# Kernel tuning notes

Hardware: AMD Instinct MI355X
Metric: run time of the kernel (lower is better)

Reference implementation:

```python
import jax, jax.numpy as jnp
import numpy as np

EMB, HID, GNN_LAYERS, N_CLASS = 1024, 300, 4, 7
B, N = 64, 64
NEG = 1e30  # mask_logic constant from the original repo


def _gru_cell(x, h, wih, whh, bih, bhh):
    # PyTorch nn.GRUCell math
    gi = x @ wih.T + bih
    gh = h @ whh.T + bhh
    i_r, i_z, i_n = jnp.split(gi, 3, axis=-1)
    h_r, h_z, h_n = jnp.split(gh, 3, axis=-1)
    r = jax.nn.sigmoid(i_r + h_r)
    z = jax.nn.sigmoid(i_z + h_z)
    n = jnp.tanh(i_n + r * h_n)
    return (1.0 - z) * n + z * h


def _build_adj_smask(speakers):
    # Vectorized get_adj_mask: utterance i attends to k in [last_same_speaker(i), i-1]
    Bz, Nu = speakers.shape
    idx = jnp.arange(Nu)
    lower = idx[None, :] < idx[:, None]                              # (N,N): k < i
    same = speakers[:, :, None] == speakers[:, None, :]              # (B,N,N)
    prev_same = same & lower[None]
    last = jnp.max(jnp.where(prev_same, idx[None, None, :], -1), axis=-1)  # (B,N)
    start = jnp.maximum(last, 0)                                     # no prior same speaker -> from 0
    valid = speakers >= 0
    adj = lower[None] & (idx[None, None, :] >= start[:, :, None]) & valid[:, :, None]
    s_mask = same & valid[:, :, None] & valid[:, None, :]
    return adj.astype(jnp.float32), s_mask.astype(jnp.float32)


def _run_layer(Hin, adj, s_mask, wq, wk, b, wr0, wr1,
               wih_c, whh_c, bih_c, bhh_c, wih_p, whh_p, bih_p, bhh_p):
    # Sequential DAG update: H1[i] = GRUc(Hin[i], M) + GRUp(M, Hin[i]),
    # M = GAT attention of Hin[i] over already-computed H1[:i].
    Bz, Nu, D = Hin.shape
    x0 = Hin[:, 0]
    z = jnp.zeros_like(x0)
    C0 = _gru_cell(x0, z, wih_c, whh_c, bih_c, bhh_c)
    P0 = _gru_cell(z, x0, wih_p, whh_p, bih_p, bhh_p)
    H1 = jnp.zeros_like(Hin).at[:, 0].set(C0 + P0)

    @jax.checkpoint
    def step(H1, inp):
        Q, a, sm, i = inp                           # Q:(B,D)  a,sm:(B,N)
        # GAT score: Linear(cat(Q,K)) split into query/key parts
        alpha = (Q @ wq)[:, None] + H1 @ wk + b      # (B,N)
        alpha = alpha - (1.0 - a) * NEG              # mask_logic (positions >= i have a=0)
        w = jax.nn.softmax(alpha, axis=-1)           # (B,N)
        V = (H1 @ wr0.T) * sm[..., None] + (H1 @ wr1.T) * (1.0 - sm[..., None])
        M = jnp.einsum('bn,bnd->bd', w, V)           # (B,D)
        C = _gru_cell(Q, M, wih_c, whh_c, bih_c, bhh_c)
        P = _gru_cell(M, Q, wih_p, whh_p, bih_p, bhh_p)
        return H1.at[:, i].set(C + P), None

    xs = (jnp.moveaxis(Hin, 1, 0)[1:], jnp.moveaxis(adj, 1, 0)[1:],
          jnp.moveaxis(s_mask, 1, 0)[1:], jnp.arange(1, Nu))
    H1, _ = jax.lax.scan(step, H1, xs)
    return H1


def setup_inputs() -> dict:
    key = jax.random.key(0)
    ks = iter(jax.random.split(key, 40))
    def rn(shape, s=0.02):
        return jax.random.normal(next(ks), shape, jnp.float32) * s
    L = GNN_LAYERS
    in_dim = HID * (L + 1) + EMB
    return dict(
        features=jax.random.normal(next(ks), (B, N, EMB), jnp.float32),
        speakers=jax.random.randint(next(ks), (B, N), 0, 2, jnp.int32),
        w_in=rn((HID, EMB)), b_in=jnp.zeros((HID,), jnp.float32),
        gat_wq=rn((L, HID)), gat_wk=rn((L, HID)), gat_b=jnp.zeros((L,), jnp.float32),
        wr0=rn((L, HID, HID)), wr1=rn((L, HID, HID)),
        wih_c=rn((L, 3 * HID, HID)), whh_c=rn((L, 3 * HID, HID)),
        bih_c=jnp.zeros((L, 3 * HID), jnp.float32), bhh_c=jnp.zeros((L, 3 * HID), jnp.float32),
        wih_p=rn((L, 3 * HID, HID)), whh_p=rn((L, 3 * HID, HID)),
        bih_p=jnp.zeros((L, 3 * HID), jnp.float32), bhh_p=jnp.zeros((L, 3 * HID), jnp.float32),
        w1=rn((HID, in_dim)), b1=jnp.zeros((HID,), jnp.float32),
        w2=rn((HID, HID)), b2=jnp.zeros((HID,), jnp.float32),
        w3=rn((N_CLASS, HID)), b3=jnp.zeros((N_CLASS,), jnp.float32),
    )


def reference(features, speakers, w_in, b_in, gat_wq, gat_wk, gat_b, wr0, wr1,
              wih_c, whh_c, bih_c, bhh_c, wih_p, whh_p, bih_p, bhh_p,
              w1, b1, w2, b2, w3, b3):
    adj, s_mask = _build_adj_smask(speakers)
    H0 = jax.nn.relu(features @ w_in.T + b_in)          # (B,N,HID)
    Hs = [H0]
    Hin = H0
    for l in range(GNN_LAYERS):
        Hin = _run_layer(Hin, adj, s_mask, gat_wq[l], gat_wk[l], gat_b[l],
                         wr0[l], wr1[l], wih_c[l], whh_c[l], bih_c[l], bhh_c[l],
                         wih_p[l], whh_p[l], bih_p[l], bhh_p[l])
        Hs.append(Hin)
    Hs.append(features)
    Hcat = jnp.concatenate(Hs, axis=2)                  # (B,N,HID*(L+1)+EMB)
    h = jax.nn.relu(Hcat @ w1.T + b1)
    h = jax.nn.relu(h @ w2.T + b2)                      # dropout is identity in eval
    logits = h @ w3.T + b3                              # (B,N,N_CLASS)
    return logits
```

## Files before the change

kernel.cpp:

```cpp
#include <hip/hip_runtime.h>
#include <hip/hip_bf16.h>

typedef _Float16 f16x2 __attribute__((ext_vector_type(2)));

#define HID 300
#define NSEQ 64
#define NROWS 4096

union U { uint4 u; f16x2 h[4]; };

__device__ __forceinline__ float sigm(float x){ return 1.f/(1.f+__expf(-x)); }

__device__ __forceinline__ float fdot2a(f16x2 a, f16x2 b, float c){
#if __has_builtin(__builtin_amdgcn_fdot2)
  return __builtin_amdgcn_fdot2(a, b, c, false);
#else
  return c + (float)a.x*(float)b.x + (float)a.y*(float)b.y;
#endif
}

__device__ __forceinline__ void xstore(float* p, float v){
  __hip_atomic_store(p, v, __ATOMIC_RELAXED, __HIP_MEMORY_SCOPE_AGENT);
}
__device__ __forceinline__ float xload(const float* p){
  return __hip_atomic_load(p, __ATOMIC_RELAXED, __HIP_MEMORY_SCOPE_AGENT);
}
__device__ __forceinline__ int xloadi(const int* p){
  return __hip_atomic_load(p, __ATOMIC_RELAXED, __HIP_MEMORY_SCOPE_AGENT);
}

#define NSYNC (3*32*16 + 3*128*2*16 + 64)

__global__ void convert_all_kernel(
    const float* __restrict__ whh_c, const float* __restrict__ wih_p,
    const float* __restrict__ wih_c, const float* __restrict__ whh_p,
    const float* __restrict__ wr0,   const float* __restrict__ wr1,
    const float* __restrict__ w_in,  const float* __restrict__ w1,
    const float* __restrict__ w2,
    f16x2* __restrict__ W_M4, f16x2* __restrict__ WrT4, f16x2* __restrict__ W_P4,
    f16x2* __restrict__ W_H4, f16x2* __restrict__ W_14, f16x2* __restrict__ W_24,
    int* __restrict__ syncc)
{
  const int NA = 4*38*1800*4;
  const int NB = 4*38*600*4;
  const int NP = 4*38*1800*4;
  const int NH = 128*300*4;
  const int N1 = 318*304*4;
  const int N2 = 38*304*4;
  const int NS = NSYNC;
  const int TOT = NA+NB+NP+NH+N1+N2+NS;
  for (int idx0 = blockIdx.x*blockDim.x + threadIdx.x; idx0 < TOT; idx0 += gridDim.x*blockDim.x){
    int idx = idx0;
    if (idx < NA){
      int l    = idx/(38*1800*4);
      int rem  = idx - l*(38*1800*4);
      int kg   = rem/(1800*4);
      int rem2 = rem - kg*(1800*4);
      int o = rem2>>2, s = rem2&3;
      int c = (kg*4+s)*2;
      float v0=0.f, v1=0.f;
      if (c < 300){
        const float* src = (o<900) ? (whh_c + ((size_t)l*900+o)*300)
                                   : (wih_p + ((size_t)l*900+(o-900))*300);
        v0 = src[c]; v1 = src[c+1];
      }
      f16x2 t; t.x=(_Float16)v0; t.y=(_Float16)v1;
      W_M4[idx] = t; continue;
    }
    idx -= NA;
    if (idx < NB){
      int l    = idx/(38*600*4);
      int rem  = idx - l*(38*600*4);
      int kg   = rem/(600*4);
      int rem2 = rem - kg*(600*4);
      int t6 = rem2>>2, s = rem2&3;
      int d = t6>>1, hh = t6&1;
      int c = (kg*4+s)*2;
      float v0=0.f, v1=0.f;
      if (c < 300){
        const float* src = hh ? (wr1 + ((size_t)l*300+d)*300)
                              : (wr0 + ((size_t)l*300+d)*300);
        v0 = src[c]; v1 = src[c+1];
      }
      f16x2 t; t.x=(_Float16)v0; t.y=(_Float16)v1;
      WrT4[idx] = t; continue;
    }
    idx -= NB;
    if (idx < NP){
      int l    = idx/(38*1800*4);
      int rem  = idx - l*(38*1800*4);
      int kg   = rem/(1800*4);
      int rem2 = rem - kg*(1800*4);
      int o = rem2>>2, s = rem2&3;
      int c = (kg*4+s)*2;
      float v0=0.f, v1=0.f;
      if (c < 300){
        const float* src = (o<900) ? (wih_c + ((size_t)l*900+o)*300)
                                   : (whh_p + ((size_t)l*900+(o-900))*300);
        v0 = src[c]; v1 = src[c+1];
      }
      f16x2 t; t.x=(_Float16)v0; t.y=(_Float16)v1;
      W_P4[idx] = t; continue;
    }
    idx -= NP;
    if (idx < NH){
      int kg  = idx/(300*4);
      int rem = idx - kg*(300*4);
      int o = rem>>2, s = rem&3;
      int c = (kg*4+s)*2;
      f16x2 t; t.x=(_Float16)w_in[(size_t)o*1024+c]; t.y=(_Float16)w_in[(size_t)o*1024+c+1];
      W_H4[idx] = t; continue;
    }
    idx -= NH;
    if (idx < N1){
      int kgg = idx/(304*4);
      int rem = idx - kgg*(304*4);
      int o = rem>>2, s = rem&3;
      int segbase, seglen, kgl;
      if (kgg < 190){ int seg = kgg/38; kgl = kgg - seg*38; segbase = seg*300; seglen = 300; }
      else { int kk = kgg-190; int sf = kk>>6; kgl = kk&63; segbase = 1500 + sf*512; seglen = 512; }
      int c = (kgl*4+s)*2;
      float v0=0.f, v1=0.f;
      if (o < 300 && c < seglen){
        v0 = w1[(size_t)o*2524 + segbase + c];
        if (c+1 < seglen) v1 = w1[(size_t)o*2524 + segbase + c + 1];
      }
      f16x2 t; t.x=(_Float16)v0; t.y=(_Float16)v1;
      W_14[idx] = t; continue;
    }
    idx -= N1;
    if (idx < N2){
      int kg = idx/(304*4);
      int rem = idx - kg*(304*4);
      int o = rem>>2, s = rem&3;
      int c = (kg*4+s)*2;
      float v0=0.f, v1=0.f;
      if (o < 300 && c < 300){ v0 = w2[(size_t)o*300+c]; v1 = w2[(size_t)o*300+c+1]; }
      f16x2 t; t.x=(_Float16)v0; t.y=(_Float16)v1;
      W_24[idx] = t; continue;
    }
    idx -= N2;
    syncc[idx] = 0;
  }
}

__global__ __launch_bounds__(256) void h0_kernel(const float* __restrict__ feat,
    const f16x2* __restrict__ WH, const float* __restrict__ b_in, float* __restrict__ H0)
{
  const int tid = threadIdx.x;
  const int r0  = blockIdx.x*8;
  __shared__ f16x2 X[8][512];
  for (int t=tid; t<8*512; t+=256){
    int r=t>>9, p=t&511, c=2*p;
    f16x2 h; h.x=(_Float16)feat[(size_t)(r0+r)*1024+c];
    h.y=(_Float16)feat[(size_t)(r0+r)*1024+c+1];
    X[r][p]=h;
  }
  __syncthreads();
  const uint4* WHu = (const uint4*)WH;
  const int o0 = tid, o1 = tid+256;
  const bool h1v = (o1 < 300);
  float acc[2][8];
  #pragma unroll
  for (int j=0;j<2;j++)
    #pragma unroll
    for (int r=0;r<8;r++) acc[j][r]=0.f;
  for (int kg=0; kg<128; kg++){
    U w0, w1;
    w0.u = WHu[(size_t)kg*300 + o0];
    if (h1v) w1.u = WHu[(size_t)kg*300 + o1];
    #pragma unroll
    for (int r=0;r<8;r++){
      const f16x2* xp = &X[r][kg*4];
      f16x2 x0=xp[0],x1=xp[1],x2=xp[2],x3=xp[3];
      acc[0][r] = fdot2a(w0.h[3],x3, fdot2a(w0.h[2],x2, fdot2a(w0.h[1],x1, fdot2a(w0.h[0],x0, acc[0][r]))));
      if (h1v)
        acc[1][r] = fdot2a(w1.h[3],x3, fdot2a(w1.h[2],x2, fdot2a(w1.h[1],x1, fdot2a(w1.h[0],x0, acc[1][r]))));
    }
  }
  {
    float bb = b_in[o0];
    #pragma unroll
    for (int r=0;r<8;r++) H0[(size_t)(r0+r)*HID + o0] = fmaxf(acc[0][r]+bb, 0.f);
  }
  if (h1v){
    float bb = b_in[o1];
    #pragma unroll
    for (int r=0;r<8;r++) H0[(size_t)(r0+r)*HID + o1] = fmaxf(acc[1][r]+bb, 0.f);
  }
}

__global__ __launch_bounds__(1024) void scan_pipe_kernel(
  float* __restrict__ Hball,
  const f16x2* __restrict__ W_M4, const f16x2* __restrict__ WrT4, const f16x2* __restrict__ W_P4,
  const float* __restrict__ bih_c, const float* __restrict__ bhh_c,
  const float* __restrict__ bih_p, const float* __restrict__ bhh_p,
  const float* __restrict__ gwq, const float* __restrict__ gwk, const float* __restrict__ gbv,
  const int* __restrict__ speakers, float* __restrict__ xrow, int* __restrict__ syncc,
  float* __restrict__ xhEx)
{
  (void)gwq; (void)gbv;
  __shared__ _Float16 Hh[2][NSEQ][304];
  __shared__ float pre_s[2][1800];
  __shared__ float gates[2][1800];
  __shared__ float Mf[2][304];
  __shared__ f16x2 Mh[2][152];
  __shared__ f16x2 u01h[2][304];
  __shared__ float wgt[2][NSEQ];
  __shared__ float kd[2][NSEQ];
  __shared__ float red[2][320];
  __shared__ float xf[2][304];
  __shared__ f16x2 xh[2][152];
  __shared__ int   spk[2][NSEQ];
  __shared__ int   startA[2][NSEQ];
  __shared__ int   sLayer, sPair, sHalf;

  const int tid = threadIdx.x;

  if (tid == 0){
    int xcc = 0;
    asm volatile("s_getreg_b32 %0, hwreg(HW_REG_XCC_ID)" : "=s"(xcc));
    int pref = (xcc >> 1) & 3;
    int* claimc = syncc + 3*32*16 + 3*128*2*16;
    int l = 0, p = 0, hf = 0;
    #pragma unroll 1
    for (int t=0; t<4; ++t){
      int cand = (pref + t) & 3;
      int idx = __hip_atomic_fetch_add(&claimc[cand*16], 1, __ATOMIC_RELAXED, __HIP_MEMORY_SCOPE_AGENT);
      if (idx < 64){ l = cand; p = idx>>1; hf = idx&1; break; }
    }
    sLayer = l; sPair = p; sHalf = hf;
  }
  __syncthreads();
  const int layer = sLayer;
  const int pair  = sPair;
  const int hf    = sHalf;
  const int base0 = (2*pair)*NSEQ;
  const int base1 = (2*pair+1)*NSEQ;

  const uint4* Wm4 = (const uint4*)(W_M4 + (size_t)layer*38*1800*4);
  const uint4* Wr4 = (const uint4*)(WrT4 + (size_t)layer*38*600*4);
  const uint4* Wp4 = (const uint4*)(W_P4 + (size_t)layer*38*1800*4);
  const float* HinB0 = Hball + (size_t)base0*300;
  const float* HinB1 = Hball + (size_t)base1*300;
  float* HoutB0 = Hball + ((size_t)(layer+1)*NROWS + (size_t)base0)*300;
  float* HoutB1 = Hball + ((size_t)(layer+1)*NROWS + (size_t)base1)*300;
  int* cntP = syncc + (layer*32 + pair)*16;
  int* cntC = (layer>0) ? (syncc + ((layer-1)*32 + pair)*16) : (int*)0;
  const float* xin  = xrow + (size_t)(((layer-1)*32 + pair)*2)*NSEQ*300;
  float*       xout = xrow + (size_t)((layer*32 + pair)*2)*NSEQ*300;

  const int lp = layer*32 + pair;
  float* xhMy = xhEx + ((size_t)lp*2 + hf)*600;
  const float* xhPt = xhEx + ((size_t)lp*2 + (1-hf))*600;
  int* fEmy = syncc + 1536 + (lp*2 + hf)*16;
  const int* fEpt = syncc + 1536 + (lp*2 + (1-hf))*16;

  const int w  = tid >> 6;
  const int rc = tid >> 9;
  const int rt = tid & 511;

  float bcr=0,bcz=0,bcn=0,bpr=0,bpz=0,bpn=0,wkv=0;
  if (rt < 150){
    const int de = hf*150 + rt;
    bcr=bhh_c[layer*900+de]; bcz=bhh_c[layer*900+300+de]; bcn=bhh_c[layer*900+600+de];
    bpr=bih_p[layer*900+de]; bpz=bih_p[layer*900+300+de]; bpn=bih_p[layer*900+600+de];
    wkv=gwk[layer*300+de];
  }
  float wkp=0;
  if (tid < 300){
    const int r = (tid<150)? tid : (tid-150);
    wkp = gwk[layer*300 + (1-hf)*150 + r];
  }

  int opm = 0; float ppb = 0.f;
  if (tid < 900){
    const int g = tid/150;
    const int dd = tid - g*150;
    opm = g*300 + hf*150 + dd;
    ppb = (opm<900) ? bih_c[layer*900+opm] : bhh_p[layer*900+(opm-900)];
  }

  if (tid < 64) spk[0][tid] = speakers[base0+tid];
  else if (tid < 128) spk[1][tid-64] = speakers[base1+(tid-64)];
  for (int t=tid; t<2*1800; t+=1024) ((float*)gates)[t]=0.f;
  for (int t=tid; t<2*304; t+=1024) ((float*)Mf)[t]=0.f;
  if (tid >= 128 && tid < 168){ int t=tid-128; red[t/20][300+(t%20)] = 0.f; }
  if (tid >= 168 && tid < 176){ int t=tid-168; xf[t>>2][300+(t&3)] = 0.f; }
  if (tid >= 176 && tid < 180){
    int t=tid-176; f16x2 z; z.x=(_Float16)0.f; z.y=(_Float16)0.f;
    Mh[t>>1][150+(t&1)]=z; xh[t>>1][150+(t&1)]=z;
    u01h[t>>1][150+(t&1)]=z; u01h[t>>1][302+(t&1)]=z;
  }
  __syncthreads();
  if (tid < 64){
    int s=0; for (int j=tid-1;j>=0;--j) if (spk[0][j]==spk[0][tid]){s=j;break;}
    startA[0][tid]=s;
  } else if (tid < 128){
    int t=tid-64;
    int s=0; for (int j=t-1;j>=0;--j) if (spk[1][j]==spk[1][t]){s=j;break;}
    startA[1][t]=s;
  }
  if (layer>0 && tid==0){
    while (xloadi(cntC) < 2) __builtin_amdgcn_s_sleep(8);
  }
  __syncthreads();

  for (int i=0; i<NSEQ; ++i){
    if (rt < 150){
      float x0, x1;
      if (layer==0){
        const float* Hin = rc ? HinB1 : HinB0;
        float2 v = *(const float2*)(Hin + (size_t)i*300 + 2*rt);
        x0=v.x; x1=v.y;
      } else {
        const float* xi = xin + (size_t)rc*NSEQ*300 + (size_t)i*300;
        x0 = xload(xi + 2*rt);
        x1 = xload(xi + 2*rt + 1);
      }
      xf[rc][2*rt]=x0; xf[rc][2*rt+1]=x1;
      f16x2 h; h.x=(_Float16)x0; h.y=(_Float16)x1; xh[rc][rt]=h;
    }
    __syncthreads();
    if (tid < 900){
      float aA0=0,aA1=0,aA2=0,aA3=0, aB0=0,aB1=0,aB2=0,aB3=0;
      for (int kg=0;kg<38;kg++){
        U v; v.u = Wp4[(size_t)kg*1800 + opm];
        f16x2 xA0=xh[0][kg*4+0],xA1=xh[0][kg*4+1],xA2=xh[0][kg*4+2],xA3=xh[0][kg*4+3];
        f16x2 xB0=xh[1][kg*4+0],xB1=xh[1][kg*4+1],xB2=xh[1][kg*4+2],xB3=xh[1][kg*4+3];
        aA0=fdot2a(v.h[0],xA0,aA0); aA1=fdot2a(v.h[1],xA1,aA1);
        aA2=fdot2a(v.h[2],xA2,aA2); aA3=fdot2a(v.h[3],xA3,aA3);
        aB0=fdot2a(v.h[0],xB0,aB0); aB1=fdot2a(v.h[1],xB1,aB1);
        aB2=fdot2a(v.h[2],xB2,aB2); aB3=fdot2a(v.h[3],xB3,aB3);
      }
      pre_s[0][opm] = (aA0+aA1)+(aA2+aA3) + ppb;
      pre_s[1][opm] = (aB0+aB1)+(aB2+aB3) + ppb;
    }
    __syncthreads();
    if (i > 0){
      if (tid==0){
        while (xloadi(fEpt) < i) __builtin_amdgcn_s_sleep(1);
      }
      __syncthreads();
      if (tid < 300){
        const int c = (tid<150)? 0 : 1;
        const int r = tid - c*150;
        const int pd = (1-hf)*150 + r;
        float hv = xload(xhPt + ((i-1)&1)*300 + c*150 + r);
        red[c][pd] = hv * wkp;
        Hh[c][i-1][pd] = (_Float16)hv;
      }
      __syncthreads();
      if (w==0 || w==8){
        const int c = (w==8);
        const int lane = tid & 63;
        float s = red[c][lane]+red[c][lane+64]+red[c][lane+128]+red[c][lane+192]+red[c][lane+256];
        #pragma unroll
        for (int o=32;o>0;o>>=1) s += __shfl_xor(s,o);
        if (lane==0) kd[c][i-1]=s;
        {
          const int st = startA[c][i];
          const bool in = (lane>=st) && (lane<i);
          float kv = (lane==i-1) ? s : kd[c][lane];
          float a = in ? kv : -3.0e38f;
          float m = a;
          #pragma unroll
          for (int o=32;o>0;o>>=1) m = fmaxf(m,__shfl_xor(m,o));
          float e = in ? __expf(a-m) : 0.f;
          float ss = e;
          #pragma unroll
          for (int o=32;o>0;o>>=1) ss += __shfl_xor(ss,o);
          wgt[c][lane] = e/ss;
        }
      }
      __syncthreads();
      #pragma unroll 1
      for (int pass=0; pass<2; ++pass){
        int T = tid + pass*1024;
        if (T < 1200){
          const int c = (T >= 600);
          const int t = T - c*600;
          const int d  = (t<300)? t : (t-300);
          const int wh = (t>=300);
          const int st = startA[c][i]; const int ms = spk[c][i];
          float u=0.f;
          for (int j=st;j<i;++j){
            float sel = ((spk[c][j]==ms) != (wh!=0)) ? 1.f : 0.f;
            u += sel*wgt[c][j]*(float)Hh[c][j][d];
          }
          ((_Float16*)&u01h[c][0])[(wh?304:0) + d] = (_Float16)u;
        }
      }
      __syncthreads();
      if (tid < 600){
        const int hh = tid&1;
        const f16x2* uA = (const f16x2*)&u01h[0][0] + hh*152;
        const f16x2* uB = (const f16x2*)&u01h[1][0] + hh*152;
        float a0=0,a1=0,a2=0,a3=0, b0=0,b1=0,b2=0,b3=0;
        for (int kg=0;kg<38;kg++){
          U v; v.u = Wr4[(size_t)kg*600 + tid];
          a0=fdot2a(v.h[0],uA[kg*4+0],a0); a1=fdot2a(v.h[1],uA[kg*4+1],a1);
          a2=fdot2a(v.h[2],uA[kg*4+2],a2); a3=fdot2a(v.h[3],uA[kg*4+3],a3);
          b0=fdot2a(v.h[0],uB[kg*4+0],b0); b1=fdot2a(v.h[1],uB[kg*4+1],b1);
          b2=fdot2a(v.h[2],uB[kg*4+2],b2); b3=fdot2a(v.h[3],uB[kg*4+3],b3);
        }
        float aA = (a0+a1)+(a2+a3);
        float aB = (b0+b1)+(b2+b3);
        float m2A = aA + __shfl_xor(aA,1);
        float m2B = aB + __shfl_xor(aB,1);
        if ((tid&1)==0){ Mf[0][tid>>1] = m2A; Mf[1][tid>>1] = m2B; }
        float moA = __shfl_xor(m2A,2);
        float moB = __shfl_xor(m2B,2);
        if ((tid&3)==0){
          f16x2 hA; hA.x=(_Float16)m2A; hA.y=(_Float16)moA; Mh[0][tid>>2]=hA;
          f16x2 hB; hB.x=(_Float16)m2B; hB.y=(_Float16)moB; Mh[1][tid>>2]=hB;
        }
      }
      __syncthreads();
      if (tid < 900){
        float aA0=0,aA1=0,aA2=0,aA3=0, aB0=0,aB1=0,aB2=0,aB3=0;
        for (int kg=0;kg<38;kg++){
          U v; v.u = Wm4[(size_t)kg*1800 + opm];
          f16x2 mA0=Mh[0][kg*4+0], mA1=Mh[0][kg*4+1], mA2=Mh[0][kg*4+2], mA3=Mh[0][kg*4+3];
          f16x2 mB0=Mh[1][kg*4+0], mB1=Mh[1][kg*4+1], mB2=Mh[1][kg*4+2], mB3=Mh[1][kg*4+3];
          aA0=fdot2a(v.h[0],mA0,aA0); aA1=fdot2a(v.h[1],mA1,aA1);
          aA2=fdot2a(v.h[2],mA2,aA2); aA3=fdot2a(v.h[3],mA3,aA3);
          aB0=fdot2a(v.h[0],mB0,aB0); aB1=fdot2a(v.h[1],mB1,aB1);
          aB2=fdot2a(v.h[2],mB2,aB2); aB3=fdot2a(v.h[3],mB3,aB3);
        }
        gates[0][opm] = (aA0+aA1)+(aA2+aA3);
        gates[1][opm] = (aB0+aB1)+(aB2+aB3);
      }
      __syncthreads();
    }
    if (rt < 150){
      const int de = hf*150 + rt;
      const float M = Mf[rc][de];
      const float* ps = pre_s[rc];
      const float* gs = gates[rc];
      float r  = sigm(ps[de] + gs[de] + bcr);
      float z  = sigm(ps[300+de] + gs[300+de] + bcz);
      float n  = tanhf(ps[600+de] + r*(gs[600+de]+bcn));
      float C  = (1.f-z)*n + z*M;
      float rp = sigm(gs[900+de]+bpr + ps[900+de]);
      float zp = sigm(gs[1200+de]+bpz + ps[1200+de]);
      float np = tanhf(gs[1500+de]+bpn + rp*ps[1500+de]);
      float qv = xf[rc][de];
      float P  = (1.f-zp)*np + zp*qv;
      float h  = C + P;
      Hh[rc][i][de] = (_Float16)h;
      red[rc][de] = h*wkv;
      float* Ho = rc ? HoutB1 : HoutB0;
      Ho[(size_t)i*300 + de] = h;
      xstore(xhMy + (i&1)*300 + rc*150 + rt, h);
      if (layer<3) xstore(xout + (size_t)rc*NSEQ*300 + (size_t)i*300 + de, h);
    }
    asm volatile("s_waitcnt vmcnt(0)" ::: "memory");
    __syncthreads();
    if (tid==0){
      __hip_atomic_fetch_add(fEmy, 1, __ATOMIC_RELAXED, __HIP_MEMORY_SCOPE_AGENT);
      if (layer<3) __hip_atomic_fetch_add(cntP, 1, __ATOMIC_RELAXED, __HIP_MEMORY_SCOPE_AGENT);
      if (layer>0 && i<63){
        while (xloadi(cntC) < 2*(i+2)) __builtin_amdgcn_s_sleep(8);
      }
    }
    __syncthreads();
  }
}

__global__ __launch_bounds__(256) void head_kernel(
  const float* __restrict__ H0, const float* __restrict__ Hl1,
  const float* __restrict__ Hl2, const float* __restrict__ Hl3,
  const float* __restrict__ Hl4, const float* __restrict__ feat,
  const f16x2* __restrict__ W14, const float* __restrict__ b1,
  const f16x2* __restrict__ W24, const float* __restrict__ b2,
  const float* __restrict__ w3, const float* __restrict__ b3,
  float* __restrict__ out)
{
  const int tid = threadIdx.x;
  const int r0  = blockIdx.x*16;
  __shared__ f16x2 Xh[16*256];
  __shared__ _Float16 h1h[16*304];
  __shared__ float S2[16*304];
  const uint4* W14u = (const uint4*)W14;
  const uint4* W24u = (const uint4*)W24;

  float acc0[16], acc1[16];
  #pragma unroll
  for (int r=0;r<16;r++){ acc0[r]=0.f; acc1[r]=0.f; }
  const int o  = tid;
  const int o2 = tid + 256;
  const bool has2 = (o2 < 300);

  #pragma unroll
  for (int seg=0; seg<7; seg++){
    const float* src = (seg==0)?H0:(seg==1)?Hl1:(seg==2)?Hl2:(seg==3)?Hl3:(seg==4)?Hl4:feat;
    if (seg < 5){
      for (int t=tid; t<16*152; t+=256){
        int r=t/152, p=t-r*152, c=2*p;
        float v0 = (c<300)? src[(size_t)(r0+r)*300 + c] : 0.f;
        float v1 = (c+1<300)? src[(size_t)(r0+r)*300 + c+1] : 0.f;
        f16x2 h; h.x=(_Float16)v0; h.y=(_Float16)v1;
        Xh[r*256+p] = h;
      }
    } else {
      const int cb = (seg-5)*512;
      for (int t=tid; t<16*256; t+=256){
        int r=t>>8, p=t&255;
        float v0 = src[(size_t)(r0+r)*1024 + cb + 2*p];
        float v1 = src[(size_t)(r0+r)*1024 + cb + 2*p+1];
        f16x2 h; h.x=(_Float16)v0; h.y=(_Float16)v1;
        Xh[r*256+p] = h;
      }
    }
    __syncthreads();
    const int kgs = (seg<5)?38:64;
    const int kgo = (seg<5)? seg*38 : 190+(seg-5)*64;
    if (o < 300){
      for (int kg=0; kg<kgs; kg++){
        U a, b;
        a.u = W14u[(size_t)(kgo+kg)*304 + o];
        if (has2) b.u = W14u[(size_t)(kgo+kg)*304 + o2];
        #pragma unroll
        for (int r=0;r<16;r++){
          const f16x2* xp = &Xh[r*256 + kg*4];
          float t0 = fdot2a(a.h[0], xp[0], 0.f);
          t0 = fdot2a(a.h[1], xp[1], t0);
          t0 = fdot2a(a.h[2], xp[2], t0);
          t0 = fdot2a(a.h[3], xp[3], t0);
          acc0[r] += t0;
          if (has2){
            float t1 = fdot2a(b.h[0], xp[0], 0.f);
            t1 = fdot2a(b.h[1], xp[1], t1);
            t1 = fdot2a(b.h[2], xp[2], t1);
            t1 = fdot2a(b.h[3], xp[3], t1);
            acc1[r] += t1;
          }
        }
      }
    }
    __syncthreads();
  }
  if (o < 300){
    float bb = b1[o];
    #pragma unroll
    for (int r=0;r<16;r++) h1h[r*304+o] = (_Float16)fmaxf(acc0[r]+bb, 0.f);
  }
  if (has2){
    float bb = b1[o2];
    #pragma unroll
    for (int r=0;r<16;r++) h1h[r*304+o2] = (_Float16)fmaxf(acc1[r]+bb, 0.f);
  }
  if (tid < 4){
    #pragma unroll
    for (int r=0;r<16;r++) h1h[r*304+300+tid] = (_Float16)0.f;
  }
  __syncthreads();
  #pragma unroll
  for (int r=0;r<16;r++){ acc0[r]=0.f; acc1[r]=0.f; }
  if (o < 300){
    for (int kg=0; kg<38; kg++){
      U a, b;
      a.u = W24u[(size_t)kg*304 + o];
      if (has2) b.u = W24u[(size_t)kg*304 + o2];
      #pragma unroll
      for (int r=0;r<16;r++){
        const f16x2* xp = (const f16x2*)&h1h[r*304] + kg*4;
        float t0 = fdot2a(a.h[0], xp[0], 0.f);
        t0 = fdot2a(a.h[1], xp[1], t0);
        t0 = fdot2a(a.h[2], xp[2], t0);
        t0 = fdot2a(a.h[3], xp[3], t0);
        acc0[r] += t0;
        if (has2){
          float t1 = fdot2a(b.h[0], xp[0], 0.f);
          t1 = fdot2a(b.h[1], xp[1], t1);
          t1 = fdot2a(b.h[2], xp[2], t1);
          t1 = fdot2a(b.h[3], xp[3], t1);
          acc1[r] += t1;
        }
      }
    }
  }
  __syncthreads();
  if (o < 300){
    float bb = b2[o];
    #pragma unroll
    for (int r=0;r<16;r++) S2[r*304+o] = fmaxf(acc0[r]+bb, 0.f);
  }
  if (has2){
    float bb = b2[o2];
    #pragma unroll
    for (int r=0;r<16;r++) S2[r*304+o2] = fmaxf(acc1[r]+bb, 0.f);
  }
  __syncthreads();
  if (tid < 16*7){
    int r = tid/7, c = tid - r*7;
    float s = b3[c];
    const float* wrow = w3 + (size_t)c*HID;
    for (int k=0;k<300;k++) s += wrow[k]*S2[r*304+k];
    out[(size_t)(r0+r)*7 + c] = s;
  }
}

extern "C" void kernel_launch(void* const* d_in, const int* in_sizes, int n_in,
                              void* d_out, int out_size, void* d_ws, size_t ws_size,
                              hipStream_t stream)
{
  (void)in_sizes; (void)n_in; (void)out_size; (void)ws_size;
  const float* feat  = (const float*)d_in[0];
  const int*   spk   = (const int*)d_in[1];
  const float* w_in  = (const float*)d_in[2];
  const float* b_in  = (const float*)d_in[3];
  const float* gwq   = (const float*)d_in[4];
  const float* gwk   = (const float*)d_in[5];
  const float* gb    = (const float*)d_in[6];
  const float* wr0   = (const float*)d_in[7];
  const float* wr1   = (const float*)d_in[8];
  const float* wih_c = (const float*)d_in[9];
  const float* whh_c = (const float*)d_in[10];
  const float* bih_c = (const float*)d_in[11];
  const float* bhh_c = (const float*)d_in[12];
  const float* wih_p = (const float*)d_in[13];
  const float* whh_p = (const float*)d_in[14];
  const float* bih_p = (const float*)d_in[15];
  const float* bhh_p = (const float*)d_in[16];
  const float* w1    = (const float*)d_in[17];
  const float* b1    = (const float*)d_in[18];
  const float* w2    = (const float*)d_in[19];
  const float* b2    = (const float*)d_in[20];
  const float* w3    = (const float*)d_in[21];
  const float* b3    = (const float*)d_in[22];
  float* out = (float*)d_out;

  char* ws = (char*)d_ws;
  size_t off = 0;
  auto alloc = [&](size_t bytes)->void*{
    void* p = ws + off;
    off += (bytes + 255) & ~(size_t)255;
    return p;
  };
  f16x2* W_M4 = (f16x2*)alloc((size_t)4*38*1800*4 * sizeof(f16x2));
  f16x2* WrT4 = (f16x2*)alloc((size_t)4*38*600*4  * sizeof(f16x2));
  f16x2* W_P4 = (f16x2*)alloc((size_t)4*38*1800*4 * sizeof(f16x2));
  f16x2* W_H4 = (f16x2*)alloc((size_t)128*300*4   * sizeof(f16x2));
  f16x2* W_14 = (f16x2*)alloc((size_t)318*304*4   * sizeof(f16x2));
  f16x2* W_24 = (f16x2*)alloc((size_t)38*304*4    * sizeof(f16x2));
  float* Hball = (float*)alloc((size_t)5*NROWS*HID*sizeof(float));
  float* xrow  = (float*)alloc((size_t)3*64*NSEQ*HID*sizeof(float));
  int*   syncc = (int*)alloc((size_t)NSYNC*sizeof(int));
  float* xhEx  = (float*)alloc((size_t)128*2*600*sizeof(float));

  {
    const int tot = 4*38*1800*4 + 4*38*600*4 + 4*38*1800*4 + 128*300*4
                  + 318*304*4 + 38*304*4 + NSYNC;
    convert_all_kernel<<<(tot+255)/256, 256, 0, stream>>>(whh_c, wih_p, wih_c, whh_p,
        wr0, wr1, w_in, w1, w2, W_M4, WrT4, W_P4, W_H4, W_14, W_24, syncc);
  }
  h0_kernel<<<NROWS/8, 256, 0, stream>>>(feat, W_H4, b_in, Hball);

  scan_pipe_kernel<<<256, 1024, 0, stream>>>(Hball, W_M4, WrT4, W_P4,
      bih_c, bhh_c, bih_p, bhh_p, gwq, gwk, gb, spk, xrow, syncc, xhEx);

  head_kernel<<<NROWS/16, 256, 0, stream>>>(
      Hball, Hball + (size_t)NROWS*HID, Hball + (size_t)2*NROWS*HID,
      Hball + (size_t)3*NROWS*HID, Hball + (size_t)4*NROWS*HID,
      feat, W_14, b1, W_24, b2, w3, b3, out);
}
```

Baseline: 1.792 ms.

## Overlap partner handoff and attention softmax with input-projection GEMV via warp specialization

Warps 0 and 8 are dedicated to spinning on the partner-half flag, loading the exchanged hidden values, computing key scores and the masked softmax. The other 14 warps compute the input projection at the same time, and 4 leftover projection outputs are assigned to lanes of warp 0. This removes two block-wide barriers per sequence step and hides the cross-block wait behind the projection GEMV. In exchange, warp 0 now carries extra projection work, which may lengthen the critical path, and the spin-wait is done by whole wavefronts.

```diff
diff --git a/kernel.cpp b/kernel.cpp
--- a/kernel.cpp
+++ b/kernel.cpp
@@ -256,9 +256,10 @@
   int* fEmy = syncc + 1536 + (lp*2 + hf)*16;
   const int* fEpt = syncc + 1536 + (lp*2 + (1-hf))*16;
 
-  const int w  = tid >> 6;
-  const int rc = tid >> 9;
-  const int rt = tid & 511;
+  const int w    = tid >> 6;
+  const int rc   = tid >> 9;
+  const int rt   = tid & 511;
+  const int lane = tid & 63;
 
   float bcr=0,bcz=0,bcn=0,bpr=0,bpz=0,bpn=0,wkv=0;
   if (rt < 150){
@@ -267,18 +268,35 @@
     bpr=bih_p[layer*900+de]; bpz=bih_p[layer*900+300+de]; bpn=bih_p[layer*900+600+de];
     wkv=gwk[layer*300+de];
   }
-  float wkp=0;
-  if (tid < 300){
-    const int r = (tid<150)? tid : (tid-150);
-    wkp = gwk[layer*300 + (1-hf)*150 + r];
-  }
-
-  int opm = 0; float ppb = 0.f;
+  float wkp0=0, wkp1=0, wkp2=0;
+  if (w==0 || w==8){
+    const int pbase = layer*300 + (1-hf)*150;
+    wkp0 = gwk[pbase + lane];
+    wkp1 = gwk[pbase + 64 + lane];
+    if (lane < 22) wkp2 = gwk[pbase + 128 + lane];
+  }
+
+  const bool isP = (w != 0) && (w != 8);
+  int opmP = 0; float ppbP = 0.f;
+  if (isP){
+    const int pidx = (tid < 512) ? (tid - 64) : (tid - 128);
+    const int g = pidx/150;
+    const int dd = pidx - g*150;
+    opmP = g*300 + hf*150 + dd;
+    ppbP = (opmP<900) ? bih_c[layer*900+opmP] : bhh_p[layer*900+(opmP-900)];
+  }
+  int opmX = 0; float ppbX = 0.f;
+  if (w==0 && lane<4){
+    const int rr = 896 + lane;
+    opmX = 1500 + hf*150 + (rr - 750);
+    ppbX = (opmX<900) ? bih_c[layer*900+opmX] : bhh_p[layer*900+(opmX-900)];
+  }
+
+  int opm = 0;
   if (tid < 900){
     const int g = tid/150;
     const int dd = tid - g*150;
     opm = g*300 + hf*150 + dd;
-    ppb = (opm<900) ? bih_c[layer*900+opm] : bhh_p[layer*900+(opm-900)];
   }
 
   if (tid < 64) spk[0][tid] = speakers[base0+tid];
@@ -322,10 +340,11 @@
       f16x2 h; h.x=(_Float16)x0; h.y=(_Float16)x1; xh[rc][rt]=h;
     }
     __syncthreads();
-    if (tid < 900){
+
+    if (isP){
       float aA0=0,aA1=0,aA2=0,aA3=0, aB0=0,aB1=0,aB2=0,aB3=0;
       for (int kg=0;kg<38;kg++){
-        U v; v.u = Wp4[(size_t)kg*1800 + opm];
+        U v; v.u = Wp4[(size_t)kg*1800 + opmP];
         f16x2 xA0=xh[0][kg*4+0],xA1=xh[0][kg*4+1],xA2=xh[0][kg*4+2],xA3=xh[0][kg*4+3];
         f16x2 xB0=xh[1][kg*4+0],xB1=xh[1][kg*4+1],xB2=xh[1][kg*4+2],xB3=xh[1][kg*4+3];
         aA0=fdot2a(v.h[0],xA0,aA0); aA1=fdot2a(v.h[1],xA1,aA1);
@@ -333,47 +352,55 @@
         aB0=fdot2a(v.h[0],xB0,aB0); aB1=fdot2a(v.h[1],xB1,aB1);
         aB2=fdot2a(v.h[2],xB2,aB2); aB3=fdot2a(v.h[3],xB3,aB3);
       }
-      pre_s[0][opm] = (aA0+aA1)+(aA2+aA3) + ppb;
-      pre_s[1][opm] = (aB0+aB1)+(aB2+aB3) + ppb;
+      pre_s[0][opmP] = (aA0+aA1)+(aA2+aA3) + ppbP;
+      pre_s[1][opmP] = (aB0+aB1)+(aB2+aB3) + ppbP;
+    } else if (i > 0){
+      const int c = (w==8);
+      while (xloadi(fEpt) < i) __builtin_amdgcn_s_sleep(1);
+      const int par = ((i-1)&1)*300 + c*150;
+      const int pb = (1-hf)*150;
+      float hv0 = xload(xhPt + par + lane);
+      float hv1 = xload(xhPt + par + 64 + lane);
+      float hv2 = (lane<22) ? xload(xhPt + par + 128 + lane) : 0.f;
+      red[c][pb+lane] = hv0*wkp0;      Hh[c][i-1][pb+lane] = (_Float16)hv0;
+      red[c][pb+64+lane] = hv1*wkp1;   Hh[c][i-1][pb+64+lane] = (_Float16)hv1;
+      if (lane<22){ red[c][pb+128+lane] = hv2*wkp2; Hh[c][i-1][pb+128+lane] = (_Float16)hv2; }
+      float s = red[c][lane]+red[c][lane+64]+red[c][lane+128]+red[c][lane+192]+red[c][lane+256];
+      #pragma unroll
+      for (int o=32;o>0;o>>=1) s += __shfl_xor(s,o);
+      if (lane==0) kd[c][i-1]=s;
+      {
+        const int st = startA[c][i];
+        const bool in = (lane>=st) && (lane<i);
+        float kv = (lane==i-1) ? s : kd[c][lane];
+        float a = in ? kv : -3.0e38f;
+        float m = a;
+        #pragma unroll
+        for (int o=32;o>0;o>>=1) m = fmaxf(m,__shfl_xor(m,o));
+        float e = in ? __expf(a-m) : 0.f;
+        float ss = e;
+        #pragma unroll
+        for (int o=32;o>0;o>>=1) ss += __shfl_xor(ss,o);
+        wgt[c][lane] = e/ss;
+      }
+    }
+    if (w==0 && lane<4){
+      float aA0=0,aA1=0,aA2=0,aA3=0, aB0=0,aB1=0,aB2=0,aB3=0;
+      for (int kg=0;kg<38;kg++){
+        U v; v.u = Wp4[(size_t)kg*1800 + opmX];
+        f16x2 xA0=xh[0][kg*4+0],xA1=xh[0][kg*4+1],xA2=xh[0][kg*4+2],xA3=xh[0][kg*4+3];
+        f16x2 xB0=xh[1][kg*4+0],xB1=xh[1][kg*4+1],xB2=xh[1][kg*4+2],xB3=xh[1][kg*4+3];
+        aA0=fdot2a(v.h[0],xA0,aA0); aA1=fdot2a(v.h[1],xA1,aA1);
+        aA2=fdot2a(v.h[2],xA2,aA2); aA3=fdot2a(v.h[3],xA3,aA3);
+        aB0=fdot2a(v.h[0],xB0,aB0); aB1=fdot2a(v.h[1],xB1,aB1);
+        aB2=fdot2a(v.h[2],xB2,aB2); aB3=fdot2a(v.h[3],xB3,aB3);
+      }
+      pre_s[0][opmX] = (aA0+aA1)+(aA2+aA3) + ppbX;
+      pre_s[1][opmX] = (aB0+aB1)+(aB2+aB3) + ppbX;
     }
     __syncthreads();
+
     if (i > 0){
-      if (tid==0){
-        while (xloadi(fEpt) < i) __builtin_amdgcn_s_sleep(1);
-      }
-      __syncthreads();
-      if (tid < 300){
-        const int c = (tid<150)? 0 : 1;
-        const int r = tid - c*150;
-        const int pd = (1-hf)*150 + r;
-        float hv = xload(xhPt + ((i-1)&1)*300 + c*150 + r);
-        red[c][pd] = hv * wkp;
-        Hh[c][i-1][pd] = (_Float16)hv;
-      }
-      __syncthreads();
-      if (w==0 || w==8){
-        const int c = (w==8);
-        const int lane = tid & 63;
-        float s = red[c][lane]+red[c][lane+64]+red[c][lane+128]+red[c][lane+192]+red[c][lane+256];
-        #pragma unroll
-        for (int o=32;o>0;o>>=1) s += __shfl_xor(s,o);
-        if (lane==0) kd[c][i-1]=s;
-        {
-          const int st = startA[c][i];
-          const bool in = (lane>=st) && (lane<i);
-          float kv = (lane==i-1) ? s : kd[c][lane];
-          float a = in ? kv : -3.0e38f;
-          float m = a;
-          #pragma unroll
-          for (int o=32;o>0;o>>=1) m = fmaxf(m,__shfl_xor(m,o));
-          float e = in ? __expf(a-m) : 0.f;
-          float ss = e;
-          #pragma unroll
-          for (int o=32;o>0;o>>=1) ss += __shfl_xor(ss,o);
-          wgt[c][lane] = e/ss;
-        }
-      }
-      __syncthreads();
       #pragma unroll 1
       for (int pass=0; pass<2; ++pass){
         int T = tid + pass*1024;
```

Result: faster. 1.754 ms, median of 2 (-2.1%).
